# Performance work log

Measured on AMD Instinct MI355X. Metric: run time of the kernel, lower is better.

## Reference

```python
import jax, jax.numpy as jnp
import numpy as np

N_WIRES = 4
N_OPS = 50
B = 131072

# --- Fixed random gate sequence for tq.RandomLayer (default op set: RX, RY, RZ, CNOT) ---
_rng = np.random.RandomState(42)
RAND_GATES = []  # (kind, wires): kind 0=RX,1=RY,2=RZ,3=CNOT
for _ in range(N_OPS):
    k = int(_rng.randint(4))
    if k < 3:
        RAND_GATES.append((k, (int(_rng.randint(N_WIRES)),)))
    else:
        c, t = _rng.choice(N_WIRES, 2, replace=False)
        RAND_GATES.append((3, (int(c), int(t))))

# --- gate matrices (theta may be scalar or batched (B,)) ---
def rx_mat(t):
    c, s = jnp.cos(t / 2), jnp.sin(t / 2)
    return jnp.stack([jnp.stack([c + 0j, -1j * s], -1),
                      jnp.stack([-1j * s, c + 0j], -1)], -2).astype(jnp.complex64)

def ry_mat(t):
    c, s = jnp.cos(t / 2), jnp.sin(t / 2)
    return jnp.stack([jnp.stack([c, -s], -1),
                      jnp.stack([s, c], -1)], -2).astype(jnp.complex64)

def rz_mat(t):
    em = jnp.exp(-0.5j * t.astype(jnp.complex64))
    ep = jnp.exp(0.5j * t.astype(jnp.complex64))
    z = jnp.zeros_like(em)
    return jnp.stack([jnp.stack([em, z], -1),
                      jnp.stack([z, ep], -1)], -2).astype(jnp.complex64)

def crx_mat(t):
    c = jnp.cos(t / 2) + 0j
    s = -1j * jnp.sin(t / 2)
    U = jnp.eye(4, dtype=jnp.complex64)
    U = U.at[2, 2].set(c).at[3, 3].set(c).at[2, 3].set(s).at[3, 2].set(s)
    return U

H_MAT = (jnp.array([[1, 1], [1, -1]], jnp.complex64) / np.sqrt(2.0).astype(np.float32))
SX_MAT = 0.5 * jnp.array([[1 + 1j, 1 - 1j], [1 - 1j, 1 + 1j]], jnp.complex64)
CNOT_MAT = jnp.array([[1, 0, 0, 0], [0, 1, 0, 0], [0, 0, 0, 1], [0, 0, 1, 0]], jnp.complex64)

def apply_1q(state, U, wire):
    # state: (B,2,2,2,2); U: (2,2) or (B,2,2)
    ax = 1 + wire
    st = jnp.moveaxis(state, ax, -1)
    if U.ndim == 3:
        out = jnp.einsum('bij,b...j->b...i', U, st)
    else:
        out = jnp.einsum('ij,...j->...i', U, st)
    return jnp.moveaxis(out, -1, ax)

def apply_2q(state, U, w0, w1):
    # U: (4,4) acting on (w0, w1) with w0 the leading (control) wire
    a0, a1 = 1 + w0, 1 + w1
    st = jnp.moveaxis(state, (a0, a1), (-2, -1))
    sh = st.shape
    st = st.reshape(sh[:-2] + (4,))
    st = jnp.einsum('ij,...j->...i', U, st)
    st = st.reshape(sh)
    return jnp.moveaxis(st, (-2, -1), (a0, a1))

def _forward(features, rand_params, rx0, ry0, rz0, crx0, gamma, beta, W, b):
    bsz = features.shape[0]
    state = jnp.zeros((bsz, 16), jnp.complex64).at[:, 0].set(1.0).reshape(bsz, 2, 2, 2, 2)
    # --- GeneralEncoder '4x4_ryzxy': layers ry, rz, rx, ry over wires 0..3, 16 angles ---
    layer_fns = [ry_mat, rz_mat, rx_mat, ry_mat]
    for l in range(4):
        for w in range(4):
            state = apply_1q(state, layer_fns[l](features[:, 4 * l + w]), w)
    # --- RandomLayer (50 ops) ---
    p = 0
    for kind, wires in RAND_GATES:
        if kind == 0:
            state = apply_1q(state, rx_mat(rand_params[p]), wires[0]); p += 1
        elif kind == 1:
            state = apply_1q(state, ry_mat(rand_params[p]), wires[0]); p += 1
        elif kind == 2:
            state = apply_1q(state, rz_mat(rand_params[p]), wires[0]); p += 1
        else:
            state = apply_2q(state, CNOT_MAT, wires[0], wires[1])
    # --- trainable block ---
    state = apply_1q(state, rx_mat(rx0[0]), 0)
    state = apply_1q(state, ry_mat(ry0[0]), 1)
    state = apply_1q(state, rz_mat(rz0[0]), 3)
    state = apply_2q(state, crx_mat(crx0[0]), 0, 2)
    state = apply_1q(state, H_MAT, 3)
    state = apply_1q(state, SX_MAT, 2)
    state = apply_2q(state, CNOT_MAT, 3, 0)
    # --- MeasureAll PauliZ: <Z_w> per wire ---
    probs = (state.real ** 2 + state.imag ** 2).reshape(bsz, 16)
    bits = (jnp.arange(16)[:, None] >> jnp.arange(3, -1, -1)[None, :]) & 1  # (16,4), wire0=MSB
    signs = (1.0 - 2.0 * bits).astype(jnp.float32)
    ez = probs @ signs  # (B,4)
    # --- BatchNorm1d (training mode: batch stats, biased var) ---
    mu = ez.mean(0)
    var = ez.var(0)
    xh = (ez - mu) / jnp.sqrt(var + 1e-5)
    out = xh * gamma + beta
    # --- Linear(4,1) ---
    return out @ W.T + b

def setup_inputs() -> dict:
    key = jax.random.key(0)
    ks = jax.random.split(key, 8)
    two_pi = 2.0 * np.pi
    return {
        'features': jax.random.normal(ks[0], (B, 16), jnp.float32),
        'rand_params': jax.random.uniform(ks[1], (N_OPS,), jnp.float32, 0.0, two_pi),
        'rx0': jax.random.uniform(ks[2], (1,), jnp.float32, 0.0, two_pi),
        'ry0': jax.random.uniform(ks[3], (1,), jnp.float32, 0.0, two_pi),
        'rz0': jax.random.uniform(ks[4], (1,), jnp.float32, 0.0, two_pi),
        'crx0': jax.random.uniform(ks[5], (1,), jnp.float32, 0.0, two_pi),
        'gamma': jnp.ones((N_WIRES,), jnp.float32),
        'beta': jnp.zeros((N_WIRES,), jnp.float32),
        'W': jax.random.normal(ks[6], (1, N_WIRES), jnp.float32) * 0.5,
        'b': jnp.zeros((1,), jnp.float32),
    }

def reference(features, rand_params, rx0, ry0, rz0, crx0, gamma, beta, W, b):
    return _forward(features, rand_params, rx0, ry0, rz0, crx0, gamma, beta, W, b)
```

## Files before the change

kernel.cpp:

```cpp
#include <hip/hip_runtime.h>
#include <math.h>


struct CGates {
  int kind[64];
  int w0[64];
  int w1[64];
  int pidx[64];
  int ng;
};

constexpr unsigned int c_mt_next(unsigned int (&mt)[624], int& pos) {
  if (pos >= 624) {
    for (int i = 0; i < 624; ++i) {
      unsigned int y = (mt[i] & 0x80000000u) | (mt[(i + 1) % 624] & 0x7fffffffu);
      unsigned int v = mt[(i + 397) % 624] ^ (y >> 1);
      if (y & 1u) v ^= 0x9908b0dfu;
      mt[i] = v;
    }
    pos = 0;
  }
  unsigned int y = mt[pos++];
  y ^= y >> 11;
  y ^= (y << 7) & 0x9d2c5680u;
  y ^= (y << 15) & 0xefc60000u;
  y ^= y >> 18;
  return y;
}

constexpr CGates make_gates() {
  CGates gl{};
  unsigned int mt[624] = {};
  mt[0] = 42u;
  for (int i = 1; i < 624; ++i)
    mt[i] = 1812433253u * (mt[i - 1] ^ (mt[i - 1] >> 30)) + (unsigned int)i;
  int pos = 624;
  int ng = 0, p = 0;
  for (int op = 0; op < 50; ++op) {
    unsigned int k = c_mt_next(mt, pos) & 3u;
    if (k < 3u) {
      unsigned int w = c_mt_next(mt, pos) & 3u;
      gl.kind[ng] = (int)k; gl.w0[ng] = (int)w; gl.w1[ng] = 0;
      gl.pidx[ng] = p++;
      ++ng;
    } else {
      int arr[4] = {0, 1, 2, 3};
      { unsigned int j = c_mt_next(mt, pos) & 3u;
        int t = arr[3]; arr[3] = arr[j]; arr[j] = t; }
      { unsigned int j = c_mt_next(mt, pos) & 3u;
        while (j > 2u) j = c_mt_next(mt, pos) & 3u;
        int t = arr[2]; arr[2] = arr[j]; arr[j] = t; }
      { unsigned int j = c_mt_next(mt, pos) & 1u;
        int t = arr[1]; arr[1] = arr[j]; arr[j] = t; }
      gl.kind[ng] = 3; gl.w0[ng] = arr[0]; gl.w1[ng] = arr[1]; gl.pidx[ng] = -1;
      ++ng;
    }
  }
  gl.kind[ng] = 0; gl.w0[ng] = 0; gl.w1[ng] = 0; gl.pidx[ng] = -2; ++ng;
  gl.kind[ng] = 1; gl.w0[ng] = 1; gl.w1[ng] = 0; gl.pidx[ng] = -3; ++ng;
  gl.kind[ng] = 2; gl.w0[ng] = 3; gl.w1[ng] = 0; gl.pidx[ng] = -4; ++ng;
  gl.kind[ng] = 4; gl.w0[ng] = 0; gl.w1[ng] = 2; gl.pidx[ng] = -5; ++ng;
  gl.kind[ng] = 5; gl.w0[ng] = 3; gl.w1[ng] = 0; gl.pidx[ng] = -1; ++ng;
  gl.kind[ng] = 6; gl.w0[ng] = 2; gl.w1[ng] = 0; gl.pidx[ng] = -1; ++ng;
  gl.kind[ng] = 3; gl.w0[ng] = 3; gl.w1[ng] = 0; gl.pidx[ng] = -1; ++ng;
  gl.ng = ng;
  return gl;
}

inline constexpr CGates GL = make_gates();

inline constexpr int CK1 = GL.ng / 4;
inline constexpr int CK2 = GL.ng / 2;
inline constexpr int CK3 = (3 * GL.ng) / 4;


template <int TB>
__device__ __forceinline__ void ap_rx(float (&sx)[16], float (&sy)[16],
                                      float c, float s) {
#pragma unroll
  for (int i = 0; i < 16; ++i) {
    if (i & TB) continue;
    const int j = i | TB;
    float ax = sx[i], ay = sy[i], bx = sx[j], by = sy[j];
    sx[i] = c * ax + s * by;  sy[i] = c * ay - s * bx;
    sx[j] = c * bx + s * ay;  sy[j] = c * by - s * ax;
  }
}

template <int TB>
__device__ __forceinline__ void ap_ry(float (&sx)[16], float (&sy)[16],
                                      float c, float s) {
#pragma unroll
  for (int i = 0; i < 16; ++i) {
    if (i & TB) continue;
    const int j = i | TB;
    float ax = sx[i], ay = sy[i], bx = sx[j], by = sy[j];
    sx[i] = c * ax - s * bx;  sy[i] = c * ay - s * by;
    sx[j] = s * ax + c * bx;  sy[j] = s * ay + c * by;
  }
}

template <int TB>
__device__ __forceinline__ void ap_rz(float (&sx)[16], float (&sy)[16],
                                      float c, float s) {
#pragma unroll
  for (int i = 0; i < 16; ++i) {
    if (i & TB) continue;
    const int j = i | TB;
    float ax = sx[i], ay = sy[i], bx = sx[j], by = sy[j];
    sx[i] = c * ax + s * ay;  sy[i] = c * ay - s * ax;
    sx[j] = c * bx - s * by;  sy[j] = c * by + s * bx;
  }
}

template <int TB>
__device__ __forceinline__ void ap_h(float (&sx)[16], float (&sy)[16]) {
  const float r = 0.70710678118654752f;
#pragma unroll
  for (int i = 0; i < 16; ++i) {
    if (i & TB) continue;
    const int j = i | TB;
    float ax = sx[i], ay = sy[i], bx = sx[j], by = sy[j];
    sx[i] = r * (ax + bx);  sy[i] = r * (ay + by);
    sx[j] = r * (ax - bx);  sy[j] = r * (ay - by);
  }
}

template <int TB>
__device__ __forceinline__ void ap_sxg(float (&sx)[16], float (&sy)[16]) {
#pragma unroll
  for (int i = 0; i < 16; ++i) {
    if (i & TB) continue;
    const int j = i | TB;
    float ax = sx[i], ay = sy[i], bx = sx[j], by = sy[j];
    sx[i] = 0.5f * (ax - ay + bx + by);  sy[i] = 0.5f * (ay + ax + by - bx);
    sx[j] = 0.5f * (ax + ay + bx - by);  sy[j] = 0.5f * (ay - ax + by + bx);
  }
}

template <int CB, int TB>
__device__ __forceinline__ void ap_cnot(float (&sx)[16], float (&sy)[16]) {
#pragma unroll
  for (int i = 0; i < 16; ++i) {
    if (!(i & CB) || (i & TB)) continue;
    const int j = i | TB;
    float tx = sx[i], ty = sy[i];
    sx[i] = sx[j]; sy[i] = sy[j];
    sx[j] = tx;    sy[j] = ty;
  }
}

template <int CB, int TB>
__device__ __forceinline__ void ap_crx(float (&sx)[16], float (&sy)[16],
                                       float c, float s) {
#pragma unroll
  for (int i = 0; i < 16; ++i) {
    if (!(i & CB) || (i & TB)) continue;
    const int j = i | TB;
    float ax = sx[i], ay = sy[i], bx = sx[j], by = sy[j];
    sx[i] = c * ax + s * by;  sy[i] = c * ay - s * bx;
    sx[j] = c * bx + s * ay;  sy[j] = c * by - s * ax;
  }
}

template <int G, int GEND>
__device__ __forceinline__ void apply_range(
    float (&sx)[16], float (&sy)[16], const float* __restrict__ rp,
    const float* __restrict__ rx0, const float* __restrict__ ry0,
    const float* __restrict__ rz0, const float* __restrict__ crx0) {
  if constexpr (G < GEND) {
    constexpr int kind = GL.kind[G];
    constexpr int TB0 = 8 >> GL.w0[G];
    constexpr int TB1 = 8 >> GL.w1[G];
    constexpr int pi = GL.pidx[G];
    float c = 0.f, s = 0.f;
    if constexpr (kind == 0 || kind == 1 || kind == 2 || kind == 4) {
      float th;
      if constexpr (pi >= 0)       th = rp[pi];
      else if constexpr (pi == -2) th = rx0[0];
      else if constexpr (pi == -3) th = ry0[0];
      else if constexpr (pi == -4) th = rz0[0];
      else                         th = crx0[0];
      float h = 0.5f * th;
      s = __sinf(h);
      c = __cosf(h);
    }
    if constexpr (kind == 0)      ap_rx<TB0>(sx, sy, c, s);
    else if constexpr (kind == 1) ap_ry<TB0>(sx, sy, c, s);
    else if constexpr (kind == 2) ap_rz<TB0>(sx, sy, c, s);
    else if constexpr (kind == 3) ap_cnot<TB0, TB1>(sx, sy);
    else if constexpr (kind == 4) ap_crx<TB0, TB1>(sx, sy, c, s);
    else if constexpr (kind == 5) ap_h<TB0>(sx, sy);
    else                          ap_sxg<TB0>(sx, sy);
    apply_range<G + 1, GEND>(sx, sy, rp, rx0, ry0, rz0, crx0);
  }
}

__device__ __forceinline__ void phase1(const float* __restrict__ features,
                                       long long b, float (&t01x)[4],
                                       float (&t01y)[4], float (&t23x)[4],
                                       float (&t23y)[4]) {
  const float4* fp = (const float4*)(features + b * 16);
  float4 F0 = fp[0], F1 = fp[1], F2 = fp[2], F3 = fp[3];
  float L0[4] = {F0.x, F0.y, F0.z, F0.w};
  float L1[4] = {F1.x, F1.y, F1.z, F1.w};
  float L2[4] = {F2.x, F2.y, F2.z, F2.w};
  float L3[4] = {F3.x, F3.y, F3.z, F3.w};
  float vax[4], vay[4], vbx[4], vby[4];
#pragma unroll
  for (int w = 0; w < 4; ++w) {
    float h0 = 0.5f * L0[w], h1 = 0.5f * L1[w];
    float h2 = 0.5f * L2[w], h3 = 0.5f * L3[w];
    float s0 = __sinf(h0), c0 = __cosf(h0);
    float s1 = __sinf(h1), c1 = __cosf(h1);
    float s2 = __sinf(h2), c2 = __cosf(h2);
    float s3 = __sinf(h3), c3 = __cosf(h3);
    float ax = c0 * c1, ay = -c0 * s1;
    float bx = s0 * c1, by = s0 * s1;
    float a2x = c2 * ax + s2 * by, a2y = c2 * ay - s2 * bx;
    float b2x = s2 * ay + c2 * bx, b2y = -s2 * ax + c2 * by;
    vax[w] = c3 * a2x - s3 * b2x; vay[w] = c3 * a2y - s3 * b2y;
    vbx[w] = s3 * a2x + c3 * b2x; vby[w] = s3 * a2y + c3 * b2y;
  }
  t01x[0] = vax[0] * vax[1] - vay[0] * vay[1]; t01y[0] = vax[0] * vay[1] + vay[0] * vax[1];
  t01x[1] = vax[0] * vbx[1] - vay[0] * vby[1]; t01y[1] = vax[0] * vby[1] + vay[0] * vbx[1];
  t01x[2] = vbx[0] * vax[1] - vby[0] * vay[1]; t01y[2] = vbx[0] * vay[1] + vby[0] * vax[1];
  t01x[3] = vbx[0] * vbx[1] - vby[0] * vby[1]; t01y[3] = vbx[0] * vby[1] + vby[0] * vbx[1];
  t23x[0] = vax[2] * vax[3] - vay[2] * vay[3]; t23y[0] = vax[2] * vay[3] + vay[2] * vax[3];
  t23x[1] = vax[2] * vbx[3] - vay[2] * vby[3]; t23y[1] = vax[2] * vby[3] + vay[2] * vbx[3];
  t23x[2] = vbx[2] * vax[3] - vby[2] * vay[3]; t23y[2] = vbx[2] * vay[3] + vby[2] * vax[3];
  t23x[3] = vbx[2] * vbx[3] - vby[2] * vby[3]; t23y[3] = vbx[2] * vby[3] + vby[2] * vbx[3];
}

__device__ __forceinline__ void phase2(const float4* __restrict__ U4,
                                       const float (&t01x)[4], const float (&t01y)[4],
                                       const float (&t23x)[4], const float (&t23y)[4],
                                       float (&ez)[4]) {
  float sx[16], sy[16];
#pragma unroll
  for (int i = 0; i < 16; ++i) {
    int a = i >> 2, c = i & 3;
    sx[i] = t01x[a] * t23x[c] - t01y[a] * t23y[c];
    sy[i] = t01x[a] * t23y[c] + t01y[a] * t23x[c];
  }
  float e0 = 0.f, e1 = 0.f, e2 = 0.f, e3 = 0.f;
#pragma unroll
  for (int i = 0; i < 16; ++i) {
    float ax = 0.f, ay = 0.f;
#pragma unroll
    for (int j2 = 0; j2 < 8; ++j2) {
      float4 u = U4[i * 8 + j2];
      int j = 2 * j2;
      ax += u.x * sx[j] - u.y * sy[j] + u.z * sx[j + 1] - u.w * sy[j + 1];
      ay += u.x * sy[j] + u.y * sx[j] + u.z * sy[j + 1] + u.w * sx[j + 1];
    }
    float p = ax * ax + ay * ay;
    e0 += (i & 8) ? -p : p;
    e1 += (i & 4) ? -p : p;
    e2 += (i & 2) ? -p : p;
    e3 += (i & 1) ? -p : p;
  }
  ez[0] = e0; ez[1] = e1; ez[2] = e2; ez[3] = e3;
}

__global__ __launch_bounds__(256) void build_u_kernel(
    const float* __restrict__ rand_params, const float* __restrict__ rx0,
    const float* __restrict__ ry0, const float* __restrict__ rz0,
    const float* __restrict__ crx0, float2* __restrict__ U_out) {
  __shared__ float2 chunks[4][256];
  __shared__ float2 comb[2][256];
  int tid = threadIdx.x;
  int wv = tid >> 6, lane = tid & 63;

  if (lane < 16) {
    float sx[16], sy[16];
#pragma unroll
    for (int i = 0; i < 16; ++i) { sx[i] = (i == lane) ? 1.f : 0.f; sy[i] = 0.f; }
    if (wv == 0)      apply_range<0,   CK1  >(sx, sy, rand_params, rx0, ry0, rz0, crx0);
    else if (wv == 1) apply_range<CK1, CK2  >(sx, sy, rand_params, rx0, ry0, rz0, crx0);
    else if (wv == 2) apply_range<CK2, CK3  >(sx, sy, rand_params, rx0, ry0, rz0, crx0);
    else              apply_range<CK3, GL.ng>(sx, sy, rand_params, rx0, ry0, rz0, crx0);
#pragma unroll
    for (int i = 0; i < 16; ++i)
      chunks[wv][i * 16 + lane] = make_float2(sx[i], sy[i]);
  }
  __syncthreads();

  {
    int r = tid >> 4, c = tid & 15;
    float xr = 0.f, xi = 0.f, yr = 0.f, yi = 0.f;
#pragma unroll
    for (int k = 0; k < 16; ++k) {
      float2 g1 = chunks[1][r * 16 + k], g0 = chunks[0][k * 16 + c];
      xr += g1.x * g0.x - g1.y * g0.y;  xi += g1.x * g0.y + g1.y * g0.x;
      float2 g3 = chunks[3][r * 16 + k], g2 = chunks[2][k * 16 + c];
      yr += g3.x * g2.x - g3.y * g2.y;  yi += g3.x * g2.y + g3.y * g2.x;
    }
    comb[0][r * 16 + c] = make_float2(xr, xi);
    comb[1][r * 16 + c] = make_float2(yr, yi);
  }
  __syncthreads();

  {
    int r = tid >> 4, c = tid & 15;
    float ur = 0.f, ui = 0.f;
#pragma unroll
    for (int k = 0; k < 16; ++k) {
      float2 a = comb[1][r * 16 + k], d = comb[0][k * 16 + c];
      ur += a.x * d.x - a.y * d.y;
      ui += a.x * d.y + a.y * d.x;
    }
    U_out[r * 16 + c] = make_float2(ur, ui);
  }
}

__global__ __launch_bounds__(256) void main_kernel(
    const float* __restrict__ features, const float4* __restrict__ U4,
    float* __restrict__ ez_out, float* __restrict__ partials, int B, int useEz) {
  __shared__ float wred[4][8];
  int tid = threadIdx.x;

  long long b = (long long)blockIdx.x * 256 + tid;
  bool valid = b < B;
  float t01x[4], t01y[4], t23x[4], t23y[4];
  if (valid) phase1(features, b, t01x, t01y, t23x, t23y);

  float ez[4] = {0.f, 0.f, 0.f, 0.f};
  if (valid) {
    phase2(U4, t01x, t01y, t23x, t23y, ez);
    if (useEz) ((float4*)ez_out)[b] = make_float4(ez[0], ez[1], ez[2], ez[3]);
  }
  float q[8] = {ez[0], ez[1], ez[2], ez[3],
                ez[0] * ez[0], ez[1] * ez[1], ez[2] * ez[2], ez[3] * ez[3]};
#pragma unroll
  for (int off = 32; off; off >>= 1)
#pragma unroll
    for (int k = 0; k < 8; ++k) q[k] += __shfl_down(q[k], off, 64);
  int lane = tid & 63, wv = tid >> 6;
  if (lane == 0)
#pragma unroll
    for (int k = 0; k < 8; ++k) wred[wv][k] = q[k];
  __syncthreads();
  if (tid == 0) {
#pragma unroll
    for (int k = 0; k < 8; ++k)
      partials[(size_t)blockIdx.x * 8 + k] =
          wred[0][k] + wred[1][k] + wred[2][k] + wred[3][k];
  }
}

__global__ __launch_bounds__(256) void out_kernel(
    const float* __restrict__ partials, int nblk,
    const float* __restrict__ gamma, const float* __restrict__ beta,
    const float* __restrict__ W, const float* __restrict__ bias,
    const float* __restrict__ ez_in, const float* __restrict__ features,
    const float4* __restrict__ U4, float* __restrict__ out,
    int B, int useEz, float invB) {
  __shared__ float wred[4][8];
  __shared__ float coefs[5];
  int tid = threadIdx.x;

  float q[8] = {0.f, 0.f, 0.f, 0.f, 0.f, 0.f, 0.f, 0.f};
  for (int idx = tid; idx < nblk; idx += 256) {
    const float4* p4 = (const float4*)(partials + (size_t)idx * 8);
    float4 A = p4[0], Bq = p4[1];
    q[0] += A.x;  q[1] += A.y;  q[2] += A.z;  q[3] += A.w;
    q[4] += Bq.x; q[5] += Bq.y; q[6] += Bq.z; q[7] += Bq.w;
  }
#pragma unroll
  for (int off = 32; off; off >>= 1)
#pragma unroll
    for (int k = 0; k < 8; ++k) q[k] += __shfl_down(q[k], off, 64);
  int lane = tid & 63, wv = tid >> 6;
  if (lane == 0)
#pragma unroll
    for (int k = 0; k < 8; ++k) wred[wv][k] = q[k];
  __syncthreads();
  if (tid == 0) {
    float c0 = bias[0];
#pragma unroll
    for (int w = 0; w < 4; ++w) {
      float Sw = wred[0][w] + wred[1][w] + wred[2][w] + wred[3][w];
      float Qw = wred[0][4 + w] + wred[1][4 + w] + wred[2][4 + w] + wred[3][4 + w];
      float mu = Sw * invB;
      float var = Qw * invB - mu * mu;
      float inv = rsqrtf(var + 1e-5f);
      coefs[w] = W[w] * gamma[w] * inv;
      c0 += W[w] * (beta[w] - gamma[w] * mu * inv);
    }
    coefs[4] = c0;
  }
  __syncthreads();

  long long b = (long long)blockIdx.x * 256 + tid;
  if (b >= B) return;
  float ez[4];
  if (useEz) {
    float4 e = ((const float4*)ez_in)[b];
    ez[0] = e.x; ez[1] = e.y; ez[2] = e.z; ez[3] = e.w;
  } else {
    float t01x[4], t01y[4], t23x[4], t23y[4];
    phase1(features, b, t01x, t01y, t23x, t23y);
    phase2(U4, t01x, t01y, t23x, t23y, ez);
  }
  out[b] = coefs[4] + coefs[0] * ez[0] + coefs[1] * ez[1] +
           coefs[2] * ez[2] + coefs[3] * ez[3];
}

extern "C" void kernel_launch(void* const* d_in, const int* in_sizes, int n_in,
                              void* d_out, int out_size, void* d_ws, size_t ws_size,
                              hipStream_t stream) {
  const float* features    = (const float*)d_in[0];
  const float* rand_params = (const float*)d_in[1];
  const float* rx0         = (const float*)d_in[2];
  const float* ry0         = (const float*)d_in[3];
  const float* rz0         = (const float*)d_in[4];
  const float* crx0        = (const float*)d_in[5];
  const float* gamma       = (const float*)d_in[6];
  const float* beta        = (const float*)d_in[7];
  const float* W           = (const float*)d_in[8];
  const float* bias        = (const float*)d_in[9];
  float* out = (float*)d_out;

  int B = in_sizes[0] / 16;
  int nblk = (B + 255) / 256;

  char* ws = (char*)d_ws;
  float2* U = (float2*)ws;
  float* partials = (float*)(ws + 2048);
  size_t ez_off = (2048 + (size_t)nblk * 32 + 255) & ~(size_t)255;
  float* ez = (float*)(ws + ez_off);
  int useEz = (ws_size >= ez_off + (size_t)B * 16) ? 1 : 0;

  build_u_kernel<<<1, 256, 0, stream>>>(rand_params, rx0, ry0, rz0, crx0, U);
  main_kernel<<<nblk, 256, 0, stream>>>(features, (const float4*)U, ez,
                                        partials, B, useEz);
  out_kernel<<<nblk, 256, 0, stream>>>(partials, nblk, gamma, beta, W, bias,
                                       ez, features, (const float4*)U, out,
                                       B, useEz, 1.0f / (float)B);
}
```

Measured before the change: 24.18 us.

## Split each sample's 16x16 unitary apply across two threads

The main kernel now gives each batch element to a pair of threads. Each thread computes the full product state, applies half of the 16 unitary rows, and the pair combines expectation values with a shuffle-xor. The block reduction is halved to undo the double-counted sums, and launch bounds now request higher occupancy. The aim is to cut per-thread register pressure and latency and to double the number of threads in flight. The cost is redundant phase1 trig work per pair and twice as many blocks.

```diff
diff --git a/kernel.cpp b/kernel.cpp
--- a/kernel.cpp
+++ b/kernel.cpp
@@ -232,10 +232,10 @@
   t23x[3] = vbx[2] * vbx[3] - vby[2] * vby[3]; t23y[3] = vbx[2] * vby[3] + vby[2] * vbx[3];
 }
 
-__device__ __forceinline__ void phase2(const float4* __restrict__ U4,
-                                       const float (&t01x)[4], const float (&t01y)[4],
-                                       const float (&t23x)[4], const float (&t23y)[4],
-                                       float (&ez)[4]) {
+__device__ __forceinline__ void phase2_full(const float4* __restrict__ U4,
+                                            const float (&t01x)[4], const float (&t01y)[4],
+                                            const float (&t23x)[4], const float (&t23y)[4],
+                                            float (&ez)[4]) {
   float sx[16], sy[16];
 #pragma unroll
   for (int i = 0; i < 16; ++i) {
@@ -314,22 +314,51 @@
   }
 }
 
-__global__ __launch_bounds__(256) void main_kernel(
+__global__ __launch_bounds__(256, 4) void main_kernel(
     const float* __restrict__ features, const float4* __restrict__ U4,
     float* __restrict__ ez_out, float* __restrict__ partials, int B, int useEz) {
   __shared__ float wred[4][8];
   int tid = threadIdx.x;
-
-  long long b = (long long)blockIdx.x * 256 + tid;
-  bool valid = b < B;
-  float t01x[4], t01y[4], t23x[4], t23y[4];
-  if (valid) phase1(features, b, t01x, t01y, t23x, t23y);
+  int half = tid & 1;
+  long long e = (long long)blockIdx.x * 128 + (tid >> 1);
+  bool valid = e < B;
 
   float ez[4] = {0.f, 0.f, 0.f, 0.f};
   if (valid) {
-    phase2(U4, t01x, t01y, t23x, t23y, ez);
-    if (useEz) ((float4*)ez_out)[b] = make_float4(ez[0], ez[1], ez[2], ez[3]);
-  }
+    float t01x[4], t01y[4], t23x[4], t23y[4];
+    phase1(features, e, t01x, t01y, t23x, t23y);
+    float2 sv[16], nv[16];
+#pragma unroll
+    for (int i = 0; i < 16; ++i) {
+      int a = i >> 2, c = i & 3;
+      float sxv = t01x[a] * t23x[c] - t01y[a] * t23y[c];
+      float syv = t01x[a] * t23y[c] + t01y[a] * t23x[c];
+      sv[i] = make_float2(sxv, syv);
+      nv[i] = make_float2(-syv, sxv);
+    }
+    int rbase = half * 8;
+#pragma unroll
+    for (int r = 0; r < 8; ++r) {
+      int i = rbase + r;
+      float2 a = make_float2(0.f, 0.f);
+#pragma unroll
+      for (int j2 = 0; j2 < 8; ++j2) {
+        float4 u = U4[i * 8 + j2];
+        int j = 2 * j2;
+        a = a + sv[j] * u.x + nv[j] * u.y + sv[j + 1] * u.z + nv[j + 1] * u.w;
+      }
+      float p = a.x * a.x + a.y * a.y;
+      ez[0] += (i & 8) ? -p : p;
+      ez[1] += (i & 4) ? -p : p;
+      ez[2] += (i & 2) ? -p : p;
+      ez[3] += (i & 1) ? -p : p;
+    }
+  }
+#pragma unroll
+  for (int k = 0; k < 4; ++k) ez[k] += __shfl_xor(ez[k], 1, 64);
+  if (valid && useEz && half == 0)
+    ((float4*)ez_out)[e] = make_float4(ez[0], ez[1], ez[2], ez[3]);
+
   float q[8] = {ez[0], ez[1], ez[2], ez[3],
                 ez[0] * ez[0], ez[1] * ez[1], ez[2] * ez[2], ez[3] * ez[3]};
 #pragma unroll
@@ -345,7 +374,7 @@
 #pragma unroll
     for (int k = 0; k < 8; ++k)
       partials[(size_t)blockIdx.x * 8 + k] =
-          wred[0][k] + wred[1][k] + wred[2][k] + wred[3][k];
+          0.5f * (wred[0][k] + wred[1][k] + wred[2][k] + wred[3][k]);
   }
 }
 
@@ -401,7 +430,7 @@
   } else {
     float t01x[4], t01y[4], t23x[4], t23y[4];
     phase1(features, b, t01x, t01y, t23x, t23y);
-    phase2(U4, t01x, t01y, t23x, t23y, ez);
+    phase2_full(U4, t01x, t01y, t23x, t23y, ez);
   }
   out[b] = coefs[4] + coefs[0] * ez[0] + coefs[1] * ez[1] +
            coefs[2] * ez[2] + coefs[3] * ez[3];
@@ -423,19 +452,20 @@
   float* out = (float*)d_out;
 
   int B = in_sizes[0] / 16;
-  int nblk = (B + 255) / 256;
+  int nblkB = (B + 127) / 128;
+  int nblkC = (B + 255) / 256;
 
   char* ws = (char*)d_ws;
   float2* U = (float2*)ws;
   float* partials = (float*)(ws + 2048);
-  size_t ez_off = (2048 + (size_t)nblk * 32 + 255) & ~(size_t)255;
+  size_t ez_off = (2048 + (size_t)nblkB * 32 + 255) & ~(size_t)255;
   float* ez = (float*)(ws + ez_off);
   int useEz = (ws_size >= ez_off + (size_t)B * 16) ? 1 : 0;
 
   build_u_kernel<<<1, 256, 0, stream>>>(rand_params, rx0, ry0, rz0, crx0, U);
-  main_kernel<<<nblk, 256, 0, stream>>>(features, (const float4*)U, ez,
-                                        partials, B, useEz);
-  out_kernel<<<nblk, 256, 0, stream>>>(partials, nblk, gamma, beta, W, bias,
-                                       ez, features, (const float4*)U, out,
-                                       B, useEz, 1.0f / (float)B);
-}
+  main_kernel<<<nblkB, 256, 0, stream>>>(features, (const float4*)U, ez,
+                                         partials, B, useEz);
+  out_kernel<<<nblkC, 256, 0, stream>>>(partials, nblkB, gamma, beta, W, bias,
+                                        ez, features, (const float4*)U, out,
+                                        B, useEz, 1.0f / (float)B);
+}
```

Result: slower. 34.07 us (+40.9%).

## Split each sample's 16x16 unitary product across two threads

Applied to the files above, without the earlier changes.

The main kernel now assigns two threads per batch element. Each thread computes the encoded state, and each evaluates half of the rows of the precomputed 16x16 unitary. The partial expectation values are then combined through shared memory before the batch-stat reduction. A launch_bounds occupancy hint is also added. The aim is more parallelism and less per-thread register pressure in the dominant matvec. The cost is that the encoding trig is computed twice, an extra shared-memory sync is needed, and the grid doubles.

```diff
diff --git a/kernel.cpp b/kernel.cpp
--- a/kernel.cpp
+++ b/kernel.cpp
@@ -196,10 +196,9 @@
   }
 }
 
-__device__ __forceinline__ void phase1(const float* __restrict__ features,
-                                       long long b, float (&t01x)[4],
-                                       float (&t01y)[4], float (&t23x)[4],
-                                       float (&t23y)[4]) {
+__device__ __forceinline__ void enc_state(const float* __restrict__ features,
+                                          long long b, float (&sx)[16],
+                                          float (&sy)[16]) {
   const float4* fp = (const float4*)(features + b * 16);
   float4 F0 = fp[0], F1 = fp[1], F2 = fp[2], F3 = fp[3];
   float L0[4] = {F0.x, F0.y, F0.z, F0.w};
@@ -222,6 +221,7 @@
     vax[w] = c3 * a2x - s3 * b2x; vay[w] = c3 * a2y - s3 * b2y;
     vbx[w] = s3 * a2x + c3 * b2x; vby[w] = s3 * a2y + c3 * b2y;
   }
+  float t01x[4], t01y[4], t23x[4], t23y[4];
   t01x[0] = vax[0] * vax[1] - vay[0] * vay[1]; t01y[0] = vax[0] * vay[1] + vay[0] * vax[1];
   t01x[1] = vax[0] * vbx[1] - vay[0] * vby[1]; t01y[1] = vax[0] * vby[1] + vay[0] * vbx[1];
   t01x[2] = vbx[0] * vax[1] - vby[0] * vay[1]; t01y[2] = vbx[0] * vay[1] + vby[0] * vax[1];
@@ -230,37 +230,44 @@
   t23x[1] = vax[2] * vbx[3] - vay[2] * vby[3]; t23y[1] = vax[2] * vby[3] + vay[2] * vbx[3];
   t23x[2] = vbx[2] * vax[3] - vby[2] * vay[3]; t23y[2] = vbx[2] * vay[3] + vby[2] * vax[3];
   t23x[3] = vbx[2] * vbx[3] - vby[2] * vby[3]; t23y[3] = vbx[2] * vby[3] + vby[2] * vbx[3];
-}
-
-__device__ __forceinline__ void phase2(const float4* __restrict__ U4,
-                                       const float (&t01x)[4], const float (&t01y)[4],
-                                       const float (&t23x)[4], const float (&t23y)[4],
-                                       float (&ez)[4]) {
-  float sx[16], sy[16];
 #pragma unroll
   for (int i = 0; i < 16; ++i) {
     int a = i >> 2, c = i & 3;
     sx[i] = t01x[a] * t23x[c] - t01y[a] * t23y[c];
     sy[i] = t01x[a] * t23y[c] + t01y[a] * t23x[c];
   }
-  float e0 = 0.f, e1 = 0.f, e2 = 0.f, e3 = 0.f;
-#pragma unroll
-  for (int i = 0; i < 16; ++i) {
+}
+
+template <int HALF>
+__device__ __forceinline__ void phase2_half(const float4* __restrict__ U4,
+                                            const float (&sx)[16],
+                                            const float (&sy)[16],
+                                            float (&ez)[4]) {
+#pragma unroll
+  for (int r = 0; r < 8; ++r) {
+    const int i = HALF * 8 + r;
     float ax = 0.f, ay = 0.f;
 #pragma unroll
     for (int j2 = 0; j2 < 8; ++j2) {
       float4 u = U4[i * 8 + j2];
-      int j = 2 * j2;
+      const int j = 2 * j2;
       ax += u.x * sx[j] - u.y * sy[j] + u.z * sx[j + 1] - u.w * sy[j + 1];
       ay += u.x * sy[j] + u.y * sx[j] + u.z * sy[j + 1] + u.w * sx[j + 1];
     }
     float p = ax * ax + ay * ay;
-    e0 += (i & 8) ? -p : p;
-    e1 += (i & 4) ? -p : p;
-    e2 += (i & 2) ? -p : p;
-    e3 += (i & 1) ? -p : p;
-  }
-  ez[0] = e0; ez[1] = e1; ez[2] = e2; ez[3] = e3;
+    ez[0] += (i & 8) ? -p : p;
+    ez[1] += (i & 4) ? -p : p;
+    ez[2] += (i & 2) ? -p : p;
+    ez[3] += (i & 1) ? -p : p;
+  }
+}
+
+__device__ __forceinline__ void phase2_full(const float4* __restrict__ U4,
+                                            const float (&sx)[16],
+                                            const float (&sy)[16],
+                                            float (&ez)[4]) {
+  phase2_half<0>(U4, sx, sy, ez);
+  phase2_half<1>(U4, sx, sy, ez);
 }
 
 __global__ __launch_bounds__(256) void build_u_kernel(
@@ -314,22 +321,35 @@
   }
 }
 
-__global__ __launch_bounds__(256) void main_kernel(
+__global__ __launch_bounds__(256, 4) void main_kernel(
     const float* __restrict__ features, const float4* __restrict__ U4,
     float* __restrict__ ez_out, float* __restrict__ partials, int B, int useEz) {
+  __shared__ float4 ezsh[128];
   __shared__ float wred[4][8];
   int tid = threadIdx.x;
-
-  long long b = (long long)blockIdx.x * 256 + tid;
-  bool valid = b < B;
-  float t01x[4], t01y[4], t23x[4], t23y[4];
-  if (valid) phase1(features, b, t01x, t01y, t23x, t23y);
+  int half = tid >> 7;
+  int eidx = tid & 127;
+  long long e = (long long)blockIdx.x * 128 + eidx;
+  bool valid = e < B;
+
+  float ezp[4] = {0.f, 0.f, 0.f, 0.f};
+  if (valid) {
+    float sx[16], sy[16];
+    enc_state(features, e, sx, sy);
+    if (half == 0) phase2_half<0>(U4, sx, sy, ezp);
+    else           phase2_half<1>(U4, sx, sy, ezp);
+  }
+  if (half == 0) ezsh[eidx] = make_float4(ezp[0], ezp[1], ezp[2], ezp[3]);
+  __syncthreads();
 
   float ez[4] = {0.f, 0.f, 0.f, 0.f};
-  if (valid) {
-    phase2(U4, t01x, t01y, t23x, t23y, ez);
-    if (useEz) ((float4*)ez_out)[b] = make_float4(ez[0], ez[1], ez[2], ez[3]);
-  }
+  if (half == 1 && valid) {
+    float4 o = ezsh[eidx];
+    ez[0] = ezp[0] + o.x; ez[1] = ezp[1] + o.y;
+    ez[2] = ezp[2] + o.z; ez[3] = ezp[3] + o.w;
+    if (useEz) ((float4*)ez_out)[e] = make_float4(ez[0], ez[1], ez[2], ez[3]);
+  }
+
   float q[8] = {ez[0], ez[1], ez[2], ez[3],
                 ez[0] * ez[0], ez[1] * ez[1], ez[2] * ez[2], ez[3] * ez[3]};
 #pragma unroll
@@ -394,14 +414,14 @@
 
   long long b = (long long)blockIdx.x * 256 + tid;
   if (b >= B) return;
-  float ez[4];
+  float ez[4] = {0.f, 0.f, 0.f, 0.f};
   if (useEz) {
     float4 e = ((const float4*)ez_in)[b];
     ez[0] = e.x; ez[1] = e.y; ez[2] = e.z; ez[3] = e.w;
   } else {
-    float t01x[4], t01y[4], t23x[4], t23y[4];
-    phase1(features, b, t01x, t01y, t23x, t23y);
-    phase2(U4, t01x, t01y, t23x, t23y, ez);
+    float sx[16], sy[16];
+    enc_state(features, b, sx, sy);
+    phase2_full(U4, sx, sy, ez);
   }
   out[b] = coefs[4] + coefs[0] * ez[0] + coefs[1] * ez[1] +
            coefs[2] * ez[2] + coefs[3] * ez[3];
@@ -423,19 +443,20 @@
   float* out = (float*)d_out;
 
   int B = in_sizes[0] / 16;
-  int nblk = (B + 255) / 256;
+  int nblkB = (B + 127) / 128;
+  int nblkC = (B + 255) / 256;
 
   char* ws = (char*)d_ws;
   float2* U = (float2*)ws;
   float* partials = (float*)(ws + 2048);
-  size_t ez_off = (2048 + (size_t)nblk * 32 + 255) & ~(size_t)255;
+  size_t ez_off = (2048 + (size_t)nblkB * 32 + 255) & ~(size_t)255;
   float* ez = (float*)(ws + ez_off);
   int useEz = (ws_size >= ez_off + (size_t)B * 16) ? 1 : 0;
 
   build_u_kernel<<<1, 256, 0, stream>>>(rand_params, rx0, ry0, rz0, crx0, U);
-  main_kernel<<<nblk, 256, 0, stream>>>(features, (const float4*)U, ez,
-                                        partials, B, useEz);
-  out_kernel<<<nblk, 256, 0, stream>>>(partials, nblk, gamma, beta, W, bias,
-                                       ez, features, (const float4*)U, out,
-                                       B, useEz, 1.0f / (float)B);
-}
+  main_kernel<<<nblkB, 256, 0, stream>>>(features, (const float4*)U, ez,
+                                         partials, B, useEz);
+  out_kernel<<<nblkC, 256, 0, stream>>>(partials, nblkB, gamma, beta, W, bias,
+                                        ez, features, (const float4*)U, out,
+                                        B, useEz, 1.0f / (float)B);
+}
```

Result: faster. 23.44 us (-3.1%).
